# Performance work log

Measured on AMD Instinct MI355X. Metric: run time of the kernel, lower is better.

The kernel has to match this reference:

```python
import jax, jax.numpy as jnp
import numpy as np

B, L, DIM, ET, NH, SD, NC = 32, 200, 36, 128, 64, 9, 2


def setup_inputs() -> dict:
    key = jax.random.key(0)
    ks = jax.random.split(key, 16)
    f = jnp.float32
    vals = jax.random.normal(ks[0], (B, L, DIM), f)
    obs = (jax.random.uniform(ks[1], (B, L, DIM)) < 0.7).astype(f)  # 0/1 observation mask
    x = jnp.concatenate([vals, obs], -1)                            # (B, L, 2*DIM)
    time_steps = jnp.sort(jax.random.uniform(ks[2], (B, L)), axis=1)
    static_info = jax.random.normal(ks[3], (B, SD), f)
    query_param = jnp.linspace(0.0, 1.0, ET, dtype=f)               # nn.Parameter(linspace)

    def lin(k, o, i, s):
        return jax.random.normal(k, (o, i), f) * s

    return dict(
        x=x, time_steps=time_steps, static_info=static_info, query_param=query_param,
        periodic_w=lin(ks[4], ET - 1, 1, 1.0), periodic_b=jnp.zeros((ET - 1,), f),
        timelin_w=lin(ks[5], 1, 1, 1.0), timelin_b=jnp.zeros((1,), f),
        qw=lin(ks[6], ET, ET, ET ** -0.5), qb=jnp.zeros((ET,), f),
        kw=lin(ks[7], ET, ET, ET ** -0.5), kb=jnp.zeros((ET,), f),
        ow=lin(ks[8], DIM, 2 * DIM, (2 * DIM) ** -0.5), ob=jnp.zeros((DIM,), f),
        gru_w_ih=lin(ks[9], 3 * NH, DIM, DIM ** -0.5),
        gru_w_hh=lin(ks[10], 3 * NH, NH, NH ** -0.5),
        gru_b_ih=jnp.zeros((3 * NH,), f), gru_b_hh=jnp.zeros((3 * NH,), f),
        st_w=lin(ks[11], 8, SD, SD ** -0.5), st_b=jnp.zeros((8,), f),
        c1_w=lin(ks[12], NH + 8, NH + 8, (NH + 8) ** -0.5), c1_b=jnp.zeros((NH + 8,), f),
        bn_g=jnp.ones((NH + 8,), f), bn_b=jnp.zeros((NH + 8,), f),
        c2_w=lin(ks[13], NC, NH + 8, (NH + 8) ** -0.5), c2_b=jnp.zeros((NC,), f),
        rand_mask=jax.random.randint(ks[14], (B, L), 0, 2, jnp.int32),
    )


def reference(x, time_steps, static_info, query_param, periodic_w, periodic_b,
              timelin_w, timelin_b, qw, qb, kw, kb, ow, ob,
              gru_w_ih, gru_w_hh, gru_b_ih, gru_b_hh, st_w, st_b,
              c1_w, c1_b, bn_g, bn_b, c2_w, c2_b, rand_mask):
    dim = x.shape[-1] // 2
    irr = x[:, :, dim:]                                   # observation mask channels
    temp = rand_mask.astype(x.dtype)[:, :, None]          # random_masking keep-mask
    m_small = irr * temp
    irr2 = jnp.concatenate([irr, irr], -1)                # (B, L, 2*dim)
    m2 = jnp.concatenate([m_small, m_small], -1)

    def time_emb(tt):
        tt = tt[..., None]
        return jnp.concatenate([tt @ timelin_w.T + timelin_b,
                                jnp.sin(tt @ periodic_w.T + periodic_b)], -1)

    key_e = time_emb(time_steps)                          # (B, L, ET)
    query_e = time_emb(query_param[None, :])[0]           # (ET, ET)
    q = query_e @ qw.T + qb                               # num_heads=1 => dk=ET
    k = key_e @ kw.T + kb
    scores = jnp.einsum('qd,bld->bql', q, k) / jnp.sqrt(jnp.asarray(ET, x.dtype))

    def mta(mask):
        # per-channel masked softmax over keys l: (B, Lq, L, 2*dim)
        s5 = jnp.where(mask[:, None, :, :] == 0, jnp.asarray(-1e9, x.dtype),
                       scores[:, :, :, None])
        p = jax.nn.softmax(s5, axis=2)
        o = jnp.einsum('bqld,bld->bqd', p, x)             # (B, Lq, 2*dim)
        return o @ ow.T + ob                              # (B, Lq, dim)

    out_te = mta(irr2)
    out1_te = mta(m2)

    sx = x[:, :, :dim]
    sx_g = jnp.round(jax.nn.sigmoid(jnp.einsum('bld,ble->bde', sx, sx)))
    sout = jax.nn.sigmoid(jnp.einsum('bqd,bqe->bde', out_te, out_te))

    def step(h, xt):  # torch GRU cell, gate order r,z,n
        gi = xt @ gru_w_ih.T + gru_b_ih
        gh = h @ gru_w_hh.T + gru_b_hh
        ir, iz, inn = jnp.split(gi, 3, -1)
        hr, hz, hn = jnp.split(gh, 3, -1)
        r = jax.nn.sigmoid(ir + hr)
        z = jax.nn.sigmoid(iz + hz)
        n = jnp.tanh(inn + r * hn)
        return (1 - z) * n + z * h, None

    h0 = jnp.zeros((x.shape[0], gru_w_hh.shape[1]), x.dtype)
    h_fin, _ = jax.lax.scan(step, h0, jnp.swapaxes(out_te, 0, 1))

    st = static_info @ st_w.T + st_b
    cls_in = jnp.concatenate([h_fin, st], 1)
    z1 = cls_in @ c1_w.T + c1_b
    mu = z1.mean(0)
    var = z1.var(0)                                       # BatchNorm1d (training stats)
    zn = (z1 - mu) / jnp.sqrt(var + 1e-5) * bn_g + bn_b
    zg = jax.nn.gelu(zn, approximate=False)
    logits = zg @ c2_w.T + c2_b
    return (out_te, out1_te, logits, sx_g, sout, query_param)
```

## Files before the change

### kernel.cpp

```cpp
#include <hip/hip_runtime.h>

#define B_   32
#define L_   200
#define DIM_ 36
#define ET_  128
#define NH_  64
#define SD_  9
#define NC_  2

#define O_TE   0
#define O_T1   147456
#define O_LG   294912
#define O_SXG  294976
#define O_SOUT 336448
#define O_QP   377920

typedef __fp16 half_t;
typedef __attribute__((ext_vector_type(2))) __fp16 half2_t;

__device__ __forceinline__ float sigm(float x) { return 1.f / (1.f + expf(-x)); }
__device__ __forceinline__ float fsigm(float x) {
  return __builtin_amdgcn_rcpf(1.f + __expf(-x));
}
__device__ __forceinline__ float ftanh(float x) {
  return 2.f * __builtin_amdgcn_rcpf(1.f + __expf(-2.f * x)) - 1.f;
}
__device__ __forceinline__ half2_t f2h2(float a, float b) {
  return __builtin_amdgcn_cvt_pkrtz(a, b);
}
__device__ __forceinline__ float dot2acc(half2_t w, half2_t h, float acc) {
#if __has_builtin(__builtin_amdgcn_fdot2)
  return __builtin_amdgcn_fdot2(w, h, acc, false);
#else
  return acc + (float)w.x * (float)h.x + (float)w.y * (float)h.y;
#endif
}

__global__ __launch_bounds__(256) void k_pre(
    const float* __restrict__ qw, const float* __restrict__ kw,
    const float* __restrict__ qb, const float* __restrict__ qp,
    const float* __restrict__ x, float* __restrict__ M,
    float* __restrict__ xmean, float* __restrict__ out) {
  __shared__ float qs[128][17];
  __shared__ float ks[128][17];
  __shared__ __align__(16) float sxs[L_][76];
  int blk = blockIdx.x, t = threadIdx.x;

  if (blk < 64) {
    int d0 = (blk & 7) << 4, e0 = (blk >> 3) << 4;
    for (int idx = t; idx < 128 * 16; idx += 256) {
      int i = idx >> 4, c = idx & 15;
      qs[i][c] = qw[i * 128 + d0 + c];
      ks[i][c] = kw[i * 128 + e0 + c];
    }
    __syncthreads();
    int dd = t & 15, ee = t >> 4;
    float a = 0.f;
    #pragma unroll 8
    for (int i = 0; i < 128; i++) a += qs[i][dd] * ks[i][ee];
    M[(d0 + dd) * 128 + e0 + ee] = a;
    return;
  }
  if (blk == 64) {
    __shared__ float qbs[128];
    if (t < 128) qbs[t] = qb[t];
    __syncthreads();
    if (t < 128) {
      float a = 0.f;
      #pragma unroll 8
      for (int i = 0; i < 128; i++) a += qbs[i] * kw[i * 128 + t];
      M[128 * 128 + t] = a;
      out[O_QP + t] = qp[t];
    }
    return;
  }
  int b = blk - 65;
  const float4* xsrc = (const float4*)(x + (size_t)b * L_ * 72);
  for (int idx = t; idx < L_ * 18; idx += 256) {
    int l = idx / 18, c = idx % 18;
    ((float4*)&sxs[l][0])[c] = xsrc[l * 18 + c];
  }
  __syncthreads();
  if (t < 72) {
    float s = 0.f;
    #pragma unroll 8
    for (int l = 0; l < L_; l++) s += sxs[l][t];
    xmean[b * 72 + t] = s * (1.0f / L_);
  }
  for (int idx = t; idx < DIM_ * DIM_; idx += 256) {
    int d = idx / DIM_, e = idx % DIM_;
    float s = 0.f;
    #pragma unroll 8
    for (int l = 0; l < L_; l++) s += sxs[l][d] * sxs[l][e];
    out[O_SXG + (size_t)b * DIM_ * DIM_ + idx] = rintf(sigm(s));
  }
}

__global__ __launch_bounds__(128) void k_qm2(
    const float* __restrict__ qp, const float* __restrict__ pw,
    const float* __restrict__ pb, const float* __restrict__ tlw,
    const float* __restrict__ tlb, const float* __restrict__ M,
    float* __restrict__ qm2) {
  __shared__ float eq[ET_];
  int q = blockIdx.x, e = threadIdx.x;
  float t = qp[q];
  eq[e] = (e == 0) ? t * tlw[0] + tlb[0] : sinf(t * pw[e - 1] + pb[e - 1]);
  __syncthreads();
  float a = M[128 * 128 + e];
  #pragma unroll 8
  for (int d = 0; d < ET_; d++) a += eq[d] * M[d * ET_ + e];
  qm2[q * ET_ + e] = a * 0.088388347648318447f;
}

__global__ __launch_bounds__(512, 1) void k_attn(
    const float* __restrict__ qm, const float* __restrict__ ts,
    const float* __restrict__ pw, const float* __restrict__ pb,
    const float* __restrict__ tlw, const float* __restrict__ tlb,
    const float* __restrict__ x, const int* __restrict__ rm,
    const float* __restrict__ xmean, const float* __restrict__ ow,
    const float* __restrict__ ob, float* __restrict__ out) {
  __shared__ __align__(16) char Abuf[102400];
  __shared__ __align__(16) float qs[16][128];
  __shared__ __align__(16) float sc[16][200];
  __shared__ __align__(16) float owsh[DIM_][72];
  float*   ksA  = (float*)Abuf;
  half2_t* wsh2 = (half2_t*)Abuf;
  float*   sums = (float*)(Abuf + 57600);
  float*   ofr  = (float*)(Abuf + 57600 + 18432);

  int b = blockIdx.x >> 3;
  int q0 = (blockIdx.x & 7) << 4;
  int tid = threadIdx.x;

  const float4* qsrc = (const float4*)(qm + q0 * ET_);
  for (int i = tid; i < 16 * 32; i += 512) ((float4*)qs)[i] = qsrc[i];
  const float4* owsrc = (const float4*)ow;
  for (int i = tid; i < DIM_ * 18; i += 512) ((float4*)owsh)[i] = owsrc[i];
  {
    float tl_w = tlw[0], tl_b = tlb[0];
    const float* tsb = ts + b * L_;
    for (int i = tid; i < L_ * 128; i += 512) {
      int l = i >> 7, j = i & 127;
      float t = tsb[l];
      float e = (j == 0) ? t * tl_w + tl_b : __sinf(t * pw[j - 1] + pb[j - 1]);
      int blkj = (j >> 2) ^ ((l >> 2) & 7);
      ksA[(l << 7) + (blkj << 2) + (j & 3)] = e;
    }
  }
  __syncthreads();

  {
    int w = tid >> 6, lg = tid & 63;
    float acc[2][4];
    #pragma unroll
    for (int i = 0; i < 2; i++)
      #pragma unroll
      for (int j = 0; j < 4; j++) acc[i][j] = 0.f;
    const float4* ks4 = (const float4*)ksA;
    const float4* qs4 = (const float4*)qs;
    int swz = lg & 7;
    #pragma unroll 4
    for (int d4 = 0; d4 < 32; d4++) {
      int xi = d4 ^ swz;
      float4 kv[4];
      #pragma unroll
      for (int j = 0; j < 4; j++) {
        int l = 4 * lg + j; if (l > 199) l = 199;
        kv[j] = ks4[(l << 5) + xi];
      }
      #pragma unroll
      for (int i = 0; i < 2; i++) {
        float4 qv = qs4[(2 * w + i) * 32 + d4];
        #pragma unroll
        for (int j = 0; j < 4; j++)
          acc[i][j] += qv.x * kv[j].x + qv.y * kv[j].y +
                       qv.z * kv[j].z + qv.w * kv[j].w;
      }
    }
    if (lg < 50) {
      #pragma unroll
      for (int i = 0; i < 2; i++) {
        float4 v = {acc[i][0], acc[i][1], acc[i][2], acc[i][3]};
        *((float4*)(&sc[2 * w + i][4 * lg])) = v;
      }
    }
  }
  __syncthreads();

  {
    int qi = tid >> 5, li = tid & 31;
    float m = -1e30f;
    for (int l = li; l < L_; l += 32) m = fmaxf(m, sc[qi][l]);
    #pragma unroll
    for (int off = 16; off >= 1; off >>= 1) m = fmaxf(m, __shfl_xor(m, off));
    for (int l = li; l < L_; l += 32) sc[qi][l] = __expf(sc[qi][l] - m);
  }

  {
    const float2* xb2 = (const float2*)(x + (size_t)b * L_ * 72);
    const int* rmb = rm + b * L_;
    for (int i = tid; i < L_ * 72; i += 512) {
      int l = i / 72, c2 = i % 72;
      int seg = c2 / 18, fh = c2 % 18;
      float2 v = xb2[l * 36 + fh];
      float2 o = xb2[l * 36 + 18 + fh];
      float rr = (float)rmb[l];
      float w0, w1;
      if (seg == 0)      { w0 = o.x * v.x;      w1 = o.y * v.y; }
      else if (seg == 1) { w0 = o.x;            w1 = o.y; }
      else if (seg == 2) { w0 = o.x * v.x * rr; w1 = o.y * v.y * rr; }
      else               { w0 = o.x * rr;       w1 = o.y * rr; }
      wsh2[l * 72 + c2] = f2h2(w0, w1);
    }
  }
  __syncthreads();

  {
    int half = tid >> 8, tt = tid & 255;
    int qi = tt >> 4, li = tt & 15;
    int l0 = half * 100;
    float accA[8], accB[8];
    #pragma unroll
    for (int k = 0; k < 8; k++) { accA[k] = 0.f; accB[k] = 0.f; }
    const float4* wA = (const float4*)wsh2;
    #pragma unroll 2
    for (int l = l0; l < l0 + 100; l++) {
      float ev = sc[qi][l];
      float4 wa = wA[l * 18 + li];
      union { float f; half2_t h; } u0, u1, u2, u3;
      u0.f = wa.x; u1.f = wa.y; u2.f = wa.z; u3.f = wa.w;
      accA[0] += ev * (float)u0.h.x; accA[1] += ev * (float)u0.h.y;
      accA[2] += ev * (float)u1.h.x; accA[3] += ev * (float)u1.h.y;
      accA[4] += ev * (float)u2.h.x; accA[5] += ev * (float)u2.h.y;
      accA[6] += ev * (float)u3.h.x; accA[7] += ev * (float)u3.h.y;
      if (li < 2) {
        float4 wb = wA[l * 18 + 16 + li];
        union { float f; half2_t h; } b0, b1, b2, b3;
        b0.f = wb.x; b1.f = wb.y; b2.f = wb.z; b3.f = wb.w;
        accB[0] += ev * (float)b0.h.x; accB[1] += ev * (float)b0.h.y;
        accB[2] += ev * (float)b1.h.x; accB[3] += ev * (float)b1.h.y;
        accB[4] += ev * (float)b2.h.x; accB[5] += ev * (float)b2.h.y;
        accB[6] += ev * (float)b3.h.x; accB[7] += ev * (float)b3.h.y;
      }
    }
    float* sq = sums + half * 2304 + qi * 144;
    float4* sA = (float4*)(sq + 8 * li);
    sA[0] = make_float4(accA[0], accA[1], accA[2], accA[3]);
    sA[1] = make_float4(accA[4], accA[5], accA[6], accA[7]);
    if (li < 2) {
      float4* sB = (float4*)(sq + 128 + 8 * li);
      sB[0] = make_float4(accB[0], accB[1], accB[2], accB[3]);
      sB[1] = make_float4(accB[4], accB[5], accB[6], accB[7]);
    }
  }
  __syncthreads();

  const float* xm = xmean + b * 72;
  for (int idx = tid; idx < 16 * DIM_; idx += 512) {
    int qq = idx / DIM_, j = idx % DIM_;
    const float* s0 = sums + qq * 144;
    const float* s1 = sums + 2304 + qq * 144;
    float numA = s0[j] + s1[j],           denA = s0[36 + j] + s1[36 + j];
    float numB = s0[72 + j] + s1[72 + j], denB = s0[108 + j] + s1[108 + j];
    float al, ah, bl, bh;
    if (denA > 0.f) { al = numA / denA; ah = 1.f; }
    else            { al = xm[j];       ah = xm[36 + j]; }
    if (denB > 0.f) { bl = numB / denB; bh = 1.f; }
    else            { bl = xm[j];       bh = xm[36 + j]; }
    float* oq = ofr + qq * 144;
    oq[j] = al;      oq[36 + j] = ah;
    oq[72 + j] = bl; oq[108 + j] = bh;
  }
  __syncthreads();

  for (int idx = tid; idx < 16 * 72; idx += 512) {
    int qq = idx / 72, t = idx % 72;
    int v = t / DIM_, i2 = t % DIM_;
    const float4* o4 = (const float4*)(ofr + qq * 144 + v * 72);
    const float4* w4 = (const float4*)(owsh[i2]);
    float a = ob[i2];
    #pragma unroll
    for (int d4 = 0; d4 < 18; d4++) {
      float4 ov = o4[d4], wv = w4[d4];
      a += ov.x * wv.x + ov.y * wv.y + ov.z * wv.z + ov.w * wv.w;
    }
    size_t off = ((size_t)b * ET_ + q0 + qq) * DIM_ + i2;
    out[(v == 0 ? O_TE : O_T1) + off] = a;
  }
}

__global__ __launch_bounds__(256, 1) void k_sg(
    const float* __restrict__ out_ro, const float* __restrict__ wih,
    const float* __restrict__ bih, const float* __restrict__ whh,
    const float* __restrict__ bhh, float* __restrict__ hfin,
    float* __restrict__ out) {
  __shared__ __align__(16) float ote_s[ET_][DIM_];
  __shared__ float gis[ET_][3 * NH_];
  __shared__ __align__(16) half2_t hpk[NH_ / 2];
  int blk = blockIdx.x, t = threadIdx.x;

  if (blk < 32) {
    int b = blk;
    const float4* osrc = (const float4*)(out_ro + O_TE + (size_t)b * ET_ * DIM_);
    for (int idx = t; idx < ET_ * 9; idx += 256)
      ((float4*)&ote_s[0][0])[idx] = osrc[idx];
    __syncthreads();
    for (int idx = t; idx < DIM_ * DIM_; idx += 256) {
      int d = idx / DIM_, e = idx % DIM_;
      float s = 0.f;
      #pragma unroll 8
      for (int q = 0; q < ET_; q++) s += ote_s[q][d] * ote_s[q][e];
      out[O_SOUT + (size_t)b * DIM_ * DIM_ + idx] = sigm(s);
    }
    return;
  }

  int b = blk - 32;
  const float* ote = out_ro + O_TE;
  const float4* osrc = (const float4*)(ote + (size_t)b * ET_ * DIM_);
  for (int idx = t; idx < ET_ * DIM_ / 4; idx += 256)
    ((float4*)&ote_s[0][0])[idx] = osrc[idx];
  __syncthreads();

  if (t < 3 * NH_) {
    float wv[DIM_];
    const float* wrow = wih + (size_t)t * DIM_;
    #pragma unroll
    for (int d = 0; d < DIM_; d++) wv[d] = wrow[d];
    float bi = bih[t] + ((t < 2 * NH_) ? bhh[t] : 0.f);
    for (int q = 0; q < ET_; q++) {
      const float4* xr = (const float4*)ote_s[q];
      float a = bi;
      #pragma unroll
      for (int c = 0; c < 9; c++) {
        float4 xv = xr[c];
        a += xv.x * wv[4 * c] + xv.y * wv[4 * c + 1] +
             xv.z * wv[4 * c + 2] + xv.w * wv[4 * c + 3];
      }
      gis[q][t] = a;
    }
  }
  __syncthreads();
  if (t >= 64) return;

  half2_t wr[32], wz[32], wn[32];
  {
    const float2* r0 = (const float2*)(whh + (size_t)t * NH_);
    const float2* r1 = (const float2*)(whh + (size_t)(NH_ + t) * NH_);
    const float2* r2 = (const float2*)(whh + (size_t)(2 * NH_ + t) * NH_);
    #pragma unroll
    for (int c = 0; c < 32; c++) {
      float2 a = r0[c], bb = r1[c], cc = r2[c];
      wr[c] = f2h2(a.x, a.y);
      wz[c] = f2h2(bb.x, bb.y);
      wn[c] = f2h2(cc.x, cc.y);
    }
  }
  float bh_n = bhh[2 * NH_ + t];

  float h = 0.f;
  ((half_t*)hpk)[t] = (half_t)0.f;
  for (int q = 0; q < ET_; q++) {
    float gi_r = gis[q][t];
    float gi_z = gis[q][NH_ + t];
    float gi_n = gis[q][2 * NH_ + t];
    float ar = 0.f, az = 0.f, an = 0.f;
    const float4* hp4 = (const float4*)hpk;
    #pragma unroll
    for (int c4 = 0; c4 < 8; c4++) {
      float4 hv = hp4[c4];
      union { float f; half2_t h; } u0, u1, u2, u3;
      u0.f = hv.x; u1.f = hv.y; u2.f = hv.z; u3.f = hv.w;
      int c = c4 * 4;
      ar = dot2acc(wr[c + 0], u0.h, ar);
      az = dot2acc(wz[c + 0], u0.h, az);
      an = dot2acc(wn[c + 0], u0.h, an);
      ar = dot2acc(wr[c + 1], u1.h, ar);
      az = dot2acc(wz[c + 1], u1.h, az);
      an = dot2acc(wn[c + 1], u1.h, an);
      ar = dot2acc(wr[c + 2], u2.h, ar);
      az = dot2acc(wz[c + 2], u2.h, az);
      an = dot2acc(wn[c + 2], u2.h, an);
      ar = dot2acc(wr[c + 3], u3.h, ar);
      az = dot2acc(wz[c + 3], u3.h, az);
      an = dot2acc(wn[c + 3], u3.h, an);
    }
    float r = fsigm(gi_r + ar);
    float z = fsigm(gi_z + az);
    float n = ftanh(gi_n + r * (an + bh_n));
    h = n + z * (h - n);
    ((half_t*)hpk)[t] = (half_t)h;
  }
  hfin[b * NH_ + t] = h;
}

__global__ __launch_bounds__(256) void k_cls(
    const float* __restrict__ hfin, const float* __restrict__ si,
    const float* __restrict__ stw, const float* __restrict__ stb,
    const float* __restrict__ c1w, const float* __restrict__ c1b,
    const float* __restrict__ bng, const float* __restrict__ bnb,
    const float* __restrict__ c2w, const float* __restrict__ c2b,
    float* __restrict__ out) {
  __shared__ float cin[B_][72];
  __shared__ float z1[B_][72];
  __shared__ float zg[B_][72];
  int t = threadIdx.x;
  for (int idx = t; idx < B_ * 8; idx += 256) {
    int b = idx / 8, j = idx % 8;
    float acc = stb[j];
    #pragma unroll
    for (int d = 0; d < SD_; d++) acc += si[b * SD_ + d] * stw[j * SD_ + d];
    cin[b][NH_ + j] = acc;
  }
  for (int idx = t; idx < B_ * NH_; idx += 256)
    cin[idx / NH_][idx % NH_] = hfin[idx];
  __syncthreads();
  for (int idx = t; idx < B_ * 72; idx += 256) {
    int b = idx / 72, j = idx % 72;
    float acc = c1b[j];
    #pragma unroll 8
    for (int d = 0; d < 72; d++) acc += cin[b][d] * c1w[j * 72 + d];
    z1[b][j] = acc;
  }
  __syncthreads();
  if (t < 72) {
    float mu = 0.f;
    for (int b = 0; b < B_; b++) mu += z1[b][t];
    mu *= (1.f / B_);
    float vv = 0.f;
    for (int b = 0; b < B_; b++) { float d = z1[b][t] - mu; vv += d * d; }
    vv *= (1.f / B_);
    float inv = 1.f / sqrtf(vv + 1e-5f);
    float g = bng[t], bb = bnb[t];
    for (int b = 0; b < B_; b++) {
      float zn = (z1[b][t] - mu) * inv * g + bb;
      zg[b][t] = 0.5f * zn * (1.f + erff(zn * 0.70710678118654752f));
    }
  }
  __syncthreads();
  for (int idx = t; idx < B_ * NC_; idx += 256) {
    int b = idx / NC_, c = idx % NC_;
    float acc = c2b[c];
    #pragma unroll 8
    for (int d = 0; d < 72; d++) acc += zg[b][d] * c2w[c * 72 + d];
    out[O_LG + idx] = acc;
  }
}

extern "C" void kernel_launch(void* const* d_in, const int* in_sizes, int n_in,
                              void* d_out, int out_size, void* d_ws,
                              size_t ws_size, hipStream_t stream) {
  const float* x    = (const float*)d_in[0];
  const float* ts   = (const float*)d_in[1];
  const float* si   = (const float*)d_in[2];
  const float* qp   = (const float*)d_in[3];
  const float* pw   = (const float*)d_in[4];
  const float* pb   = (const float*)d_in[5];
  const float* tlw  = (const float*)d_in[6];
  const float* tlb  = (const float*)d_in[7];
  const float* qw   = (const float*)d_in[8];
  const float* qb   = (const float*)d_in[9];
  const float* kw   = (const float*)d_in[10];
  const float* ow   = (const float*)d_in[12];
  const float* ob   = (const float*)d_in[13];
  const float* wih  = (const float*)d_in[14];
  const float* whh  = (const float*)d_in[15];
  const float* bih  = (const float*)d_in[16];
  const float* bhh  = (const float*)d_in[17];
  const float* stw  = (const float*)d_in[18];
  const float* stb  = (const float*)d_in[19];
  const float* c1w  = (const float*)d_in[20];
  const float* c1b  = (const float*)d_in[21];
  const float* bng  = (const float*)d_in[22];
  const float* bnb  = (const float*)d_in[23];
  const float* c2w  = (const float*)d_in[24];
  const float* c2b  = (const float*)d_in[25];
  const int*   rm   = (const int*)d_in[26];

  float* out = (float*)d_out;

  float* W = (float*)d_ws;
  float* ws_qm2   = W;
  float* ws_M     = W + 16384;
  float* ws_xmean = W + 32896;
  float* ws_hfin  = W + 35200;

  hipLaunchKernelGGL(k_pre, dim3(97), dim3(256), 0, stream,
                     qw, kw, qb, qp, x, ws_M, ws_xmean, out);
  hipLaunchKernelGGL(k_qm2, dim3(ET_), dim3(128), 0, stream,
                     qp, pw, pb, tlw, tlb, ws_M, ws_qm2);
  hipLaunchKernelGGL(k_attn, dim3(B_ * 8), dim3(512), 0, stream,
                     ws_qm2, ts, pw, pb, tlw, tlb, x, rm, ws_xmean, ow, ob,
                     out);
  hipLaunchKernelGGL(k_sg, dim3(64), dim3(256), 0, stream,
                     out, wih, bih, whh, bhh, ws_hfin, out);
  hipLaunchKernelGGL(k_cls, dim3(1), dim3(256), 0, stream,
                     ws_hfin, si, stw, stb, c1w, c1b, bng, bnb, c2w, c2b,
                     out);
}
```

Measured before the change: 263.7 us.

## Double k_attn block to 1024 threads and re-split score and PV loops

Raises the attention kernel's block size from 512 to 1024 threads. The work is re-partitioned to match: the score phase splits the sequence into two halves per query pair, softmax uses 64 lanes per query, and the weighted-sum phase splits the sequence into four quarters. The partial sums buffer is enlarged and reduced over four slices. The intent is more latency hiding and shorter per-thread loops, since there is only one block per CU. The cost is tighter register limits per thread and extra shared memory for the partials.

Measured after the change: 250.2 us. 5.1% less time.

```diff
diff --git a/kernel.cpp b/kernel.cpp
--- a/kernel.cpp
+++ b/kernel.cpp
@@ -112,34 +112,34 @@
   qm2[q * ET_ + e] = a * 0.088388347648318447f;
 }
 
-__global__ __launch_bounds__(512, 1) void k_attn(
+__global__ __launch_bounds__(1024, 1) void k_attn(
     const float* __restrict__ qm, const float* __restrict__ ts,
     const float* __restrict__ pw, const float* __restrict__ pb,
     const float* __restrict__ tlw, const float* __restrict__ tlb,
     const float* __restrict__ x, const int* __restrict__ rm,
     const float* __restrict__ xmean, const float* __restrict__ ow,
     const float* __restrict__ ob, float* __restrict__ out) {
-  __shared__ __align__(16) char Abuf[102400];
+  __shared__ __align__(16) char Abuf[103936];
   __shared__ __align__(16) float qs[16][128];
   __shared__ __align__(16) float sc[16][200];
   __shared__ __align__(16) float owsh[DIM_][72];
   float*   ksA  = (float*)Abuf;
   half2_t* wsh2 = (half2_t*)Abuf;
   float*   sums = (float*)(Abuf + 57600);
-  float*   ofr  = (float*)(Abuf + 57600 + 18432);
+  float*   ofr  = (float*)(Abuf + 57600 + 36864);
 
   int b = blockIdx.x >> 3;
   int q0 = (blockIdx.x & 7) << 4;
   int tid = threadIdx.x;
 
   const float4* qsrc = (const float4*)(qm + q0 * ET_);
-  for (int i = tid; i < 16 * 32; i += 512) ((float4*)qs)[i] = qsrc[i];
+  for (int i = tid; i < 16 * 32; i += 1024) ((float4*)qs)[i] = qsrc[i];
   const float4* owsrc = (const float4*)ow;
-  for (int i = tid; i < DIM_ * 18; i += 512) ((float4*)owsh)[i] = owsrc[i];
+  for (int i = tid; i < DIM_ * 18; i += 1024) ((float4*)owsh)[i] = owsrc[i];
   {
     float tl_w = tlw[0], tl_b = tlb[0];
     const float* tsb = ts + b * L_;
-    for (int i = tid; i < L_ * 128; i += 512) {
+    for (int i = tid; i < L_ * 128; i += 1024) {
       int l = i >> 7, j = i & 127;
       float t = tsb[l];
       float e = (j == 0) ? t * tl_w + tl_b : __sinf(t * pw[j - 1] + pb[j - 1]);
@@ -151,55 +151,59 @@
 
   {
     int w = tid >> 6, lg = tid & 63;
-    float acc[2][4];
+    int qp2 = w >> 1;
+    int lh = w & 1;
+    float acc[2][2];
     #pragma unroll
     for (int i = 0; i < 2; i++)
       #pragma unroll
-      for (int j = 0; j < 4; j++) acc[i][j] = 0.f;
+      for (int j = 0; j < 2; j++) acc[i][j] = 0.f;
     const float4* ks4 = (const float4*)ksA;
     const float4* qs4 = (const float4*)qs;
-    int swz = lg & 7;
+    int lbase = 100 * lh + 2 * lg;
+    int swz0 = (lbase >> 2) & 7;
+    int swz1 = ((lbase + 1) >> 2) & 7;
     #pragma unroll 4
     for (int d4 = 0; d4 < 32; d4++) {
-      int xi = d4 ^ swz;
-      float4 kv[4];
-      #pragma unroll
-      for (int j = 0; j < 4; j++) {
-        int l = 4 * lg + j; if (l > 199) l = 199;
-        kv[j] = ks4[(l << 5) + xi];
+      float4 kv[2];
+      {
+        int l0c = (lbase < 100 * lh + 100) ? lbase : (100 * lh + 99);
+        int l1c = (lbase + 1 < 100 * lh + 100) ? lbase + 1 : (100 * lh + 99);
+        kv[0] = ks4[(l0c << 5) + (d4 ^ swz0)];
+        kv[1] = ks4[(l1c << 5) + (d4 ^ swz1)];
       }
       #pragma unroll
       for (int i = 0; i < 2; i++) {
-        float4 qv = qs4[(2 * w + i) * 32 + d4];
+        float4 qv = qs4[(2 * qp2 + i) * 32 + d4];
         #pragma unroll
-        for (int j = 0; j < 4; j++)
+        for (int j = 0; j < 2; j++)
           acc[i][j] += qv.x * kv[j].x + qv.y * kv[j].y +
                        qv.z * kv[j].z + qv.w * kv[j].w;
       }
     }
-    if (lg < 50) {
+    if (2 * lg < 100) {
       #pragma unroll
       for (int i = 0; i < 2; i++) {
-        float4 v = {acc[i][0], acc[i][1], acc[i][2], acc[i][3]};
-        *((float4*)(&sc[2 * w + i][4 * lg])) = v;
+        float2 v = {acc[i][0], acc[i][1]};
+        *((float2*)(&sc[2 * qp2 + i][lbase])) = v;
       }
     }
   }
   __syncthreads();
 
   {
-    int qi = tid >> 5, li = tid & 31;
+    int qi = tid >> 6, li = tid & 63;
     float m = -1e30f;
-    for (int l = li; l < L_; l += 32) m = fmaxf(m, sc[qi][l]);
-    #pragma unroll
-    for (int off = 16; off >= 1; off >>= 1) m = fmaxf(m, __shfl_xor(m, off));
-    for (int l = li; l < L_; l += 32) sc[qi][l] = __expf(sc[qi][l] - m);
+    for (int l = li; l < L_; l += 64) m = fmaxf(m, sc[qi][l]);
+    #pragma unroll
+    for (int off = 32; off >= 1; off >>= 1) m = fmaxf(m, __shfl_xor(m, off));
+    for (int l = li; l < L_; l += 64) sc[qi][l] = __expf(sc[qi][l] - m);
   }
 
   {
     const float2* xb2 = (const float2*)(x + (size_t)b * L_ * 72);
     const int* rmb = rm + b * L_;
-    for (int i = tid; i < L_ * 72; i += 512) {
+    for (int i = tid; i < L_ * 72; i += 1024) {
       int l = i / 72, c2 = i % 72;
       int seg = c2 / 18, fh = c2 % 18;
       float2 v = xb2[l * 36 + fh];
@@ -216,15 +220,15 @@
   __syncthreads();
 
   {
-    int half = tid >> 8, tt = tid & 255;
+    int quarter = tid >> 8, tt = tid & 255;
     int qi = tt >> 4, li = tt & 15;
-    int l0 = half * 100;
+    int l0 = quarter * 50;
     float accA[8], accB[8];
     #pragma unroll
     for (int k = 0; k < 8; k++) { accA[k] = 0.f; accB[k] = 0.f; }
     const float4* wA = (const float4*)wsh2;
     #pragma unroll 2
-    for (int l = l0; l < l0 + 100; l++) {
+    for (int l = l0; l < l0 + 50; l++) {
       float ev = sc[qi][l];
       float4 wa = wA[l * 18 + li];
       union { float f; half2_t h; } u0, u1, u2, u3;
@@ -243,7 +247,7 @@
         accB[6] += ev * (float)b3.h.x; accB[7] += ev * (float)b3.h.y;
       }
     }
-    float* sq = sums + half * 2304 + qi * 144;
+    float* sq = sums + quarter * 2304 + qi * 144;
     float4* sA = (float4*)(sq + 8 * li);
     sA[0] = make_float4(accA[0], accA[1], accA[2], accA[3]);
     sA[1] = make_float4(accA[4], accA[5], accA[6], accA[7]);
@@ -256,12 +260,16 @@
   __syncthreads();
 
   const float* xm = xmean + b * 72;
-  for (int idx = tid; idx < 16 * DIM_; idx += 512) {
+  for (int idx = tid; idx < 16 * DIM_; idx += 1024) {
     int qq = idx / DIM_, j = idx % DIM_;
     const float* s0 = sums + qq * 144;
-    const float* s1 = sums + 2304 + qq * 144;
-    float numA = s0[j] + s1[j],           denA = s0[36 + j] + s1[36 + j];
-    float numB = s0[72 + j] + s1[72 + j], denB = s0[108 + j] + s1[108 + j];
+    const float* s1 = s0 + 2304;
+    const float* s2 = s1 + 2304;
+    const float* s3 = s2 + 2304;
+    float numA = (s0[j] + s1[j]) + (s2[j] + s3[j]);
+    float denA = (s0[36 + j] + s1[36 + j]) + (s2[36 + j] + s3[36 + j]);
+    float numB = (s0[72 + j] + s1[72 + j]) + (s2[72 + j] + s3[72 + j]);
+    float denB = (s0[108 + j] + s1[108 + j]) + (s2[108 + j] + s3[108 + j]);
     float al, ah, bl, bh;
     if (denA > 0.f) { al = numA / denA; ah = 1.f; }
     else            { al = xm[j];       ah = xm[36 + j]; }
@@ -273,7 +281,7 @@
   }
   __syncthreads();
 
-  for (int idx = tid; idx < 16 * 72; idx += 512) {
+  for (int idx = tid; idx < 16 * 72; idx += 1024) {
     int qq = idx / 72, t = idx % 72;
     int v = t / DIM_, i2 = t % DIM_;
     const float4* o4 = (const float4*)(ofr + qq * 144 + v * 72);
@@ -489,7 +497,7 @@
                      qw, kw, qb, qp, x, ws_M, ws_xmean, out);
   hipLaunchKernelGGL(k_qm2, dim3(ET_), dim3(128), 0, stream,
                      qp, pw, pb, tlw, tlb, ws_M, ws_qm2);
-  hipLaunchKernelGGL(k_attn, dim3(B_ * 8), dim3(512), 0, stream,
+  hipLaunchKernelGGL(k_attn, dim3(B_ * 8), dim3(1024), 0, stream,
                      ws_qm2, ts, pw, pb, tlw, tlb, x, rm, ws_xmean, ow, ob,
                      out);
   hipLaunchKernelGGL(k_sg, dim3(64), dim3(256), 0, stream,
```
